# Kernel tuning notes

Hardware: AMD Instinct MI355X
Metric: run time of the kernel (lower is better)

## Reference

```python
import jax, jax.numpy as jnp
import numpy as np

B, S, D_IN, D_OUT = 4, 2048, 1024, 1024

def setup_inputs() -> dict:
    key = jax.random.key(0)
    ks = jax.random.split(key, 6)
    s = 1.0 / np.sqrt(D_IN)
    return {
        "inputs": jax.random.normal(ks[0], (B, S, D_IN), dtype=jnp.float32),
        "Wq": jax.random.normal(ks[1], (D_IN, D_OUT), dtype=jnp.float32) * s,
        "Wk": jax.random.normal(ks[2], (D_IN, D_OUT), dtype=jnp.float32) * s,
        "Wv": jax.random.normal(ks[3], (D_IN, D_OUT), dtype=jnp.float32) * s,
        "Wo": jax.random.normal(ks[4], (D_OUT, D_OUT), dtype=jnp.float32) * (1.0 / np.sqrt(D_OUT)),
        "bo": jax.random.normal(ks[5], (D_OUT,), dtype=jnp.float32) * 0.01,
    }

def reference(inputs, Wq, Wk, Wv, Wo, bo):
    # QKV projections (no bias, matching qkv_bias=False)
    q = inputs @ Wq  # [B,S,D]
    k = inputs @ Wk
    v = inputs @ Wv
    # naive full attention: scores [B,S,S]
    scores = jnp.einsum('bqd,bkd->bqk', q, k) / jnp.sqrt(jnp.asarray(k.shape[-1], q.dtype))
    attn = jax.nn.softmax(scores, axis=-1)
    out = jnp.einsum('bqk,bkd->bqd', attn, v)
    return out @ Wo + bo
```

## Files before the change

### kernel.cpp

```cpp
#include <hip/hip_runtime.h>
#include <hip/hip_bf16.h>
#include <cstdint>

typedef __attribute__((ext_vector_type(8))) __bf16 bf16x8;
typedef __attribute__((ext_vector_type(4))) float  f32x4;

__device__ __forceinline__ unsigned short f2bf(float x) {
    union { float f; unsigned u; } v; v.f = x;
    unsigned r = v.u + 0x7fffu + ((v.u >> 16) & 1u);
    return (unsigned short)(r >> 16);
}
__device__ __forceinline__ unsigned pack2bf(float a, float b) {
    return (unsigned)f2bf(a) | ((unsigned)f2bf(b) << 16);
}

__device__ __forceinline__ void gld_lds16(const unsigned short* g, unsigned short* l) {
    __builtin_amdgcn_global_load_lds(
        (const __attribute__((address_space(1))) unsigned int*)g,
        (__attribute__((address_space(3))) unsigned int*)l,
        16, 0, 0);
}

__global__ void cvt_kernel(const float* __restrict__ in, unsigned short* __restrict__ out, int n4) {
    int i = blockIdx.x * blockDim.x + threadIdx.x;
    if (i < n4) {
        float4 f = ((const float4*)in)[i];
        ushort4 o;
        o.x = f2bf(f.x); o.y = f2bf(f.y); o.z = f2bf(f.z); o.w = f2bf(f.w);
        ((ushort4*)out)[i] = o;
    }
}

__global__ void wpack_kernel(const float* __restrict__ W, unsigned short* __restrict__ out) {
    int tid  = threadIdx.x;
    int lane = tid & 63;
    int chunk = blockIdx.x * 4 + (tid >> 6);
    int nt = chunk >> 5, k32 = chunk & 31;
    int r = lane & 15, q = lane >> 4;
    const float* src = W + (size_t)(k32*32 + q*8) * 1024 + nt*16 + r;
    unsigned o[4];
#pragma unroll
    for (int i = 0; i < 4; i++)
        o[i] = pack2bf(src[(size_t)(2*i) * 1024], src[(size_t)(2*i+1) * 1024]);
    *(uint4*)(out + (size_t)chunk * 512 + lane * 8) = make_uint4(o[0], o[1], o[2], o[3]);
}

__global__ void softmax_kernel(unsigned short* __restrict__ S) {
    const size_t row = blockIdx.x;
    unsigned short* p = S + row * 2048;
    const int tid = threadIdx.x;
    const int wave = tid >> 6, lane = tid & 63;

    uint4 raw = ((const uint4*)p)[tid];
    unsigned u[4] = {raw.x, raw.y, raw.z, raw.w};
    float x[8];
#pragma unroll
    for (int i = 0; i < 4; i++) {
        x[2*i]   = __uint_as_float(u[i] << 16);
        x[2*i+1] = __uint_as_float(u[i] & 0xffff0000u);
    }
    float m = x[0];
#pragma unroll
    for (int i = 1; i < 8; i++) m = fmaxf(m, x[i]);
#pragma unroll
    for (int off = 32; off >= 1; off >>= 1) m = fmaxf(m, __shfl_xor(m, off, 64));
    __shared__ float sm[4], ss[4];
    if (lane == 0) sm[wave] = m;
    __syncthreads();
    m = fmaxf(fmaxf(sm[0], sm[1]), fmaxf(sm[2], sm[3]));

    float e[8], s = 0.f;
#pragma unroll
    for (int i = 0; i < 8; i++) { e[i] = __expf(x[i] - m); s += e[i]; }
#pragma unroll
    for (int off = 32; off >= 1; off >>= 1) s += __shfl_xor(s, off, 64);
    if (lane == 0) ss[wave] = s;
    __syncthreads();
    s = ss[0] + ss[1] + ss[2] + ss[3];
    float inv = 1.0f / s;

    unsigned o[4];
#pragma unroll
    for (int i = 0; i < 4; i++)
        o[i] = pack2bf(e[2*i] * inv, e[2*i+1] * inv);
    ((uint4*)p)[tid] = make_uint4(o[0], o[1], o[2], o[3]);
}

template<int EPI>
__global__ __launch_bounds__(256)
void gemm_pk(const unsigned short* __restrict__ A, const unsigned short* __restrict__ Bpk,
             void* __restrict__ C, unsigned short* __restrict__ Ck, unsigned short* __restrict__ Cv,
             const float* __restrict__ bias,
             int lda, int ldc, int KS, int nk2, float scale,
             long long sA, long long sB, long long sC)
{
    constexpr int SMEM = (EPI == 2) ? 34816 : 32768;
    __shared__ __align__(16) char smem[SMEM];

    const int tid  = threadIdx.x;
    const int lane = tid & 63;
    const int wave = tid >> 6;
    const int bz = blockIdx.z;
    A   += (size_t)bz * sA;
    Bpk += (size_t)bz * sB;
    const int bm = blockIdx.y * 128;
    const int bn = blockIdx.x * 128;

    const int srow = tid >> 2;
    const int scol = ((tid & 3) ^ ((tid >> 3) & 3)) * 8;
    const unsigned short* pa0 = A + (size_t)(bm + srow) * lda + scol;
    const unsigned short* pa1 = pa0 + 32;
    const unsigned short* pa2 = A + (size_t)(bm + 64 + srow) * lda + scol;
    const unsigned short* pa3 = pa2 + 32;

    const int wm = (wave & 1) * 64;
    const int wn = (wave >> 1) * 64;
    const int ln15 = lane & 15;
    const int quad = lane >> 4;
    const int fko = (quad ^ ((ln15 >> 1) & 3)) * 8;
    const int ldsoff = tid * 16;

    const unsigned short* pb[4];
#pragma unroll
    for (int j = 0; j < 4; j++)
        pb[j] = Bpk + (size_t)(((bn + wn + j*16) >> 4) * KS) * 512 + lane * 8;

    f32x4 acc[4][4];
#pragma unroll
    for (int i = 0; i < 4; i++)
#pragma unroll
        for (int j = 0; j < 4; j++) acc[i][j] = (f32x4){0.f, 0.f, 0.f, 0.f};

    auto stage_issue = [&](int p, bf16x8* br) {
        char* base = smem + p * 16384;
        gld_lds16(pa0, (unsigned short*)(base + ldsoff));
        gld_lds16(pa2, (unsigned short*)(base + 4096  + ldsoff));
        gld_lds16(pa1, (unsigned short*)(base + 8192  + ldsoff));
        gld_lds16(pa3, (unsigned short*)(base + 12288 + ldsoff));
        pa0 += 64; pa1 += 64; pa2 += 64; pa3 += 64;
#pragma unroll
        for (int j = 0; j < 4; j++) {
            br[j]     = *(const bf16x8*)(pb[j]);
            br[4 + j] = *(const bf16x8*)(pb[j] + 512);
            pb[j] += 1024;
        }
    };
    auto stage_compute = [&](int p, const bf16x8* br) {
        const unsigned short* As = (const unsigned short*)(smem + p * 16384);
#pragma unroll
        for (int t = 0; t < 2; t++) {
            bf16x8 af[4];
#pragma unroll
            for (int i = 0; i < 4; i++)
                af[i] = *(const bf16x8*)&As[t*4096 + (wm + i*16 + ln15) * 32 + fko];
#pragma unroll
            for (int i = 0; i < 4; i++)
#pragma unroll
                for (int j = 0; j < 4; j++)
                    acc[i][j] = __builtin_amdgcn_mfma_f32_16x16x32_bf16(
                        af[i], br[t*4 + j], acc[i][j], 0, 0, 0);
        }
    };

    bf16x8 b0[8], b1[8];
    stage_issue(0, b0);
    for (int kt = 0; kt < nk2; kt += 2) {
        asm volatile("s_waitcnt vmcnt(0)" ::: "memory");
        __syncthreads();
        stage_issue(1, b1);
        stage_compute(0, b0);
        asm volatile("s_waitcnt vmcnt(0)" ::: "memory");
        __syncthreads();
        if (kt + 2 < nk2) stage_issue(0, b0);
        stage_compute(1, b1);
    }

    if (EPI == 0) {
        float bval[4];
#pragma unroll
        for (int j = 0; j < 4; j++) bval[j] = bias[bn + wn + j*16 + ln15];
        float* Co = (float*)C + (size_t)bz * sC;
#pragma unroll
        for (int i = 0; i < 4; i++) {
            int r0 = bm + wm + i*16 + quad*4;
#pragma unroll
            for (int j = 0; j < 4; j++) {
                int c = bn + wn + j*16 + ln15;
#pragma unroll
                for (int r = 0; r < 4; r++)
                    Co[(size_t)(r0 + r) * ldc + c] = acc[i][j][r] * scale + bval[j];
            }
        }
    } else if (EPI == 1) {
        __syncthreads();
        float* ep = (float*)(smem + wave * 4352);
        unsigned short* Co = (unsigned short*)C + (size_t)bz * sC;
#pragma unroll
        for (int i = 0; i < 4; i++) {
#pragma unroll
            for (int j = 0; j < 4; j++)
#pragma unroll
                for (int r = 0; r < 4; r++)
                    ep[(quad*4 + r) * 68 + j*16 + ln15] = acc[i][j][r] * scale;
            __builtin_amdgcn_s_waitcnt(0);
#pragma unroll
            for (int p = 0; p < 2; p++) {
                int lrow = p*8 + (lane >> 3);
                int col0 = (lane & 7) * 8;
                float4 lo = *(const float4*)&ep[lrow * 68 + col0];
                float4 hi = *(const float4*)&ep[lrow * 68 + col0 + 4];
                uint4 o;
                o.x = pack2bf(lo.x, lo.y); o.y = pack2bf(lo.z, lo.w);
                o.z = pack2bf(hi.x, hi.y); o.w = pack2bf(hi.z, hi.w);
                *(uint4*)&Co[(size_t)(bm + wm + i*16 + lrow) * ldc + bn + wn + col0] = o;
            }
            __builtin_amdgcn_s_waitcnt(0);
        }
    } else {
        __syncthreads();
        float* ep = (float*)(smem + wave * 8704);
        const int region = bn >> 10;
#pragma unroll
        for (int half = 0; half < 2; half++) {
#pragma unroll
            for (int ii = 0; ii < 2; ii++) {
                int i = half*2 + ii;
#pragma unroll
                for (int j = 0; j < 4; j++)
#pragma unroll
                    for (int r = 0; r < 4; r++)
                        ep[(ii*16 + quad*4 + r) * 68 + j*16 + ln15] = acc[i][j][r] * scale;
            }
            __builtin_amdgcn_s_waitcnt(0);
            const int mrow0 = bm + wm + half*32;
            if (region == 0) {
                unsigned short* Q = (unsigned short*)C;
#pragma unroll
                for (int p = 0; p < 4; p++) {
                    int lrow = p*8 + (lane >> 3);
                    int col0 = (lane & 7) * 8;
                    float4 lo = *(const float4*)&ep[lrow * 68 + col0];
                    float4 hi = *(const float4*)&ep[lrow * 68 + col0 + 4];
                    uint4 o;
                    o.x = pack2bf(lo.x, lo.y); o.y = pack2bf(lo.z, lo.w);
                    o.z = pack2bf(hi.x, hi.y); o.w = pack2bf(hi.z, hi.w);
                    *(uint4*)&Q[(size_t)(mrow0 + lrow) * ldc + bn + wn + col0] = o;
                }
            } else if (region == 1) {
#pragma unroll
                for (int mt = 0; mt < 2; mt++)
#pragma unroll
                    for (int c = 0; c < 2; c++) {
                        float4 f0 = *(const float4*)&ep[(mt*16 + ln15) * 68 + c*32 + quad*8];
                        float4 f1 = *(const float4*)&ep[(mt*16 + ln15) * 68 + c*32 + quad*8 + 4];
                        uint4 o;
                        o.x = pack2bf(f0.x, f0.y); o.y = pack2bf(f0.z, f0.w);
                        o.z = pack2bf(f1.x, f1.y); o.w = pack2bf(f1.z, f1.w);
                        int cid = ((mrow0 + mt*16) >> 4) * 32 + ((bn - 1024 + wn + c*32) >> 5);
                        *(uint4*)(Ck + (size_t)cid * 512 + lane * 8) = o;
                    }
            } else {
                int s32 = mrow0 >> 5;
#pragma unroll
                for (int dt = 0; dt < 4; dt++) {
                    float v[8];
#pragma unroll
                    for (int e = 0; e < 8; e++)
                        v[e] = ep[(quad*8 + e) * 68 + dt*16 + ln15];
                    uint4 o;
                    o.x = pack2bf(v[0], v[1]); o.y = pack2bf(v[2], v[3]);
                    o.z = pack2bf(v[4], v[5]); o.w = pack2bf(v[6], v[7]);
                    int cid = (((bn - 2048 + wn) >> 4) + dt) * 256 + s32;
                    *(uint4*)(Cv + (size_t)cid * 512 + lane * 8) = o;
                }
            }
            __builtin_amdgcn_s_waitcnt(0);
        }
    }
}

extern "C" void kernel_launch(void* const* d_in, const int* in_sizes, int n_in,
                              void* d_out, int out_size, void* d_ws, size_t ws_size,
                              hipStream_t stream) {
    const float* X  = (const float*)d_in[0];
    const float* Wq = (const float*)d_in[1];
    const float* Wk = (const float*)d_in[2];
    const float* Wv = (const float*)d_in[3];
    const float* Wo = (const float*)d_in[4];
    const float* bo = (const float*)d_in[5];
    float* out = (float*)d_out;

    size_t off = 0;
    auto alloc = [&](size_t bytes) {
        void* p = (char*)d_ws + off;
        off += (bytes + 255) & ~(size_t)255;
        return p;
    };
    unsigned short* Xbf  = (unsigned short*)alloc(8192ull * 1024 * 2);
    unsigned short* Wpk  = (unsigned short*)alloc(192ull * 32 * 512 * 2);
    unsigned short* Wopk = (unsigned short*)alloc(64ull * 32 * 512 * 2);
    unsigned short* Qrm  = (unsigned short*)alloc(8192ull * 1024 * 2);
    unsigned short* Kpk  = (unsigned short*)alloc(512ull * 32 * 512 * 2);
    unsigned short* Vpk  = (unsigned short*)alloc(64ull * 256 * 512 * 2);
    unsigned short* Sc   = (unsigned short*)alloc(4ull * 2048 * 2048 * 2);
    unsigned short* AO   = Xbf;

    cvt_kernel<<<(8192*1024/4 + 255)/256, 256, 0, stream>>>(X, Xbf, 8192*1024/4);
    wpack_kernel<<<512, 256, 0, stream>>>(Wq, Wpk);
    wpack_kernel<<<512, 256, 0, stream>>>(Wk, Wpk + 64*32*512);
    wpack_kernel<<<512, 256, 0, stream>>>(Wv, Wpk + 128*32*512);
    wpack_kernel<<<512, 256, 0, stream>>>(Wo, Wopk);

    gemm_pk<2><<<dim3(3072/128, 8192/128, 1), 256, 0, stream>>>(
        Xbf, Wpk, Qrm, Kpk, Vpk, nullptr, 1024, 1024, 32, 16, 1.0f, 0, 0, 0);

    gemm_pk<1><<<dim3(2048/128, 2048/128, 4), 256, 0, stream>>>(
        Qrm, Kpk, Sc, nullptr, nullptr, nullptr, 1024, 2048, 32, 16, 0.03125f,
        2048ll*1024, 128ll*32*512, 2048ll*2048);

    softmax_kernel<<<8192, 256, 0, stream>>>(Sc);

    gemm_pk<1><<<dim3(1024/128, 2048/128, 4), 256, 0, stream>>>(
        Sc, Vpk, AO, nullptr, nullptr, nullptr, 2048, 1024, 256, 32, 1.0f,
        2048ll*2048, 64ll*512, 2048ll*1024);

    gemm_pk<0><<<dim3(1024/128, 8192/128, 1), 256, 0, stream>>>(
        AO, Wopk, out, nullptr, nullptr, bo, 1024, 1024, 32, 16, 1.0f, 0, 0, 0);

    (void)n_in; (void)in_sizes; (void)out_size; (void)ws_size;
}
```

Before: 304.3 us.

## Enlarge GEMM tiles to 256x128 with 512 threads, triple-buffered LDS pipeline and swizzled blocks

The GEMM kernel now uses 8 waves per block over a 256x128 output tile. A-tiles are loaded through a three-stage LDS ring buffer with partial vmcnt waits and split barriers, and MFMA sections are wrapped in s_setprio. Block indices are remapped with an 8-way swizzle to improve L2 reuse across neighbouring blocks. This aims to hide global-load latency and cut barrier stalls, at the cost of 96KB of LDS per block, which limits occupancy and may cause tail imbalance with fewer blocks.

```diff
diff --git a/kernel.cpp b/kernel.cpp
--- a/kernel.cpp
+++ b/kernel.cpp
@@ -87,15 +87,14 @@
 }
 
 template<int EPI>
-__global__ __launch_bounds__(256)
+__global__ __launch_bounds__(512, 2)
 void gemm_pk(const unsigned short* __restrict__ A, const unsigned short* __restrict__ Bpk,
              void* __restrict__ C, unsigned short* __restrict__ Ck, unsigned short* __restrict__ Cv,
              const float* __restrict__ bias,
-             int lda, int ldc, int KS, int nk2, float scale,
+             int lda, int ldc, int KS, int ns, float scale,
              long long sA, long long sB, long long sC)
 {
-    constexpr int SMEM = (EPI == 2) ? 34816 : 32768;
-    __shared__ __align__(16) char smem[SMEM];
+    __shared__ __align__(16) char smem[98304];
 
     const int tid  = threadIdx.x;
     const int lane = tid & 63;
@@ -103,21 +102,27 @@
     const int bz = blockIdx.z;
     A   += (size_t)bz * sA;
     Bpk += (size_t)bz * sB;
-    const int bm = blockIdx.y * 128;
-    const int bn = blockIdx.x * 128;
+
+    const int gx = gridDim.x;
+    int lin = blockIdx.y * gx + blockIdx.x;
+    int cpx = (gx * gridDim.y) >> 3;
+    int swz = (lin & 7) * cpx + (lin >> 3);
+    const int bm = (swz / gx) * 256;
+    const int bn = (swz % gx) * 128;
 
     const int srow = tid >> 2;
     const int scol = ((tid & 3) ^ ((tid >> 3) & 3)) * 8;
     const unsigned short* pa0 = A + (size_t)(bm + srow) * lda + scol;
     const unsigned short* pa1 = pa0 + 32;
-    const unsigned short* pa2 = A + (size_t)(bm + 64 + srow) * lda + scol;
+    const unsigned short* pa2 = A + (size_t)(bm + 128 + srow) * lda + scol;
     const unsigned short* pa3 = pa2 + 32;
 
-    const int wm = (wave & 1) * 64;
-    const int wn = (wave >> 1) * 64;
+    const int wm = (wave & 3) * 64;
+    const int wn = (wave >> 2) * 64;
     const int ln15 = lane & 15;
     const int quad = lane >> 4;
     const int fko = (quad ^ ((ln15 >> 1) & 3)) * 8;
+    const int rbase = (wm >> 7) * 4096 + (wm & 127) * 32;
     const int ldsoff = tid * 16;
 
     const unsigned short* pb[4];
@@ -131,13 +136,15 @@
 #pragma unroll
         for (int j = 0; j < 4; j++) acc[i][j] = (f32x4){0.f, 0.f, 0.f, 0.f};
 
-    auto stage_issue = [&](int p, bf16x8* br) {
-        char* base = smem + p * 16384;
+    auto dma = [&](int buf) {
+        char* base = smem + buf * 32768;
         gld_lds16(pa0, (unsigned short*)(base + ldsoff));
-        gld_lds16(pa2, (unsigned short*)(base + 4096  + ldsoff));
-        gld_lds16(pa1, (unsigned short*)(base + 8192  + ldsoff));
-        gld_lds16(pa3, (unsigned short*)(base + 12288 + ldsoff));
+        gld_lds16(pa2, (unsigned short*)(base + 8192  + ldsoff));
+        gld_lds16(pa1, (unsigned short*)(base + 16384 + ldsoff));
+        gld_lds16(pa3, (unsigned short*)(base + 24576 + ldsoff));
         pa0 += 64; pa1 += 64; pa2 += 64; pa3 += 64;
+    };
+    auto loadB = [&](bf16x8* br) {
 #pragma unroll
         for (int j = 0; j < 4; j++) {
             br[j]     = *(const bf16x8*)(pb[j]);
@@ -145,35 +152,53 @@
             pb[j] += 1024;
         }
     };
-    auto stage_compute = [&](int p, const bf16x8* br) {
-        const unsigned short* As = (const unsigned short*)(smem + p * 16384);
-#pragma unroll
-        for (int t = 0; t < 2; t++) {
-            bf16x8 af[4];
-#pragma unroll
-            for (int i = 0; i < 4; i++)
-                af[i] = *(const bf16x8*)&As[t*4096 + (wm + i*16 + ln15) * 32 + fko];
-#pragma unroll
-            for (int i = 0; i < 4; i++)
-#pragma unroll
-                for (int j = 0; j < 4; j++)
-                    acc[i][j] = __builtin_amdgcn_mfma_f32_16x16x32_bf16(
-                        af[i], br[t*4 + j], acc[i][j], 0, 0, 0);
-        }
+    auto phase = [&](const unsigned short* As, int t, const bf16x8* br) {
+        bf16x8 af[4];
+#pragma unroll
+        for (int i = 0; i < 4; i++)
+            af[i] = *(const bf16x8*)&As[t*8192 + rbase + i*512 + ln15*32 + fko];
+        __builtin_amdgcn_s_setprio(1);
+#pragma unroll
+        for (int i = 0; i < 4; i++)
+#pragma unroll
+            for (int j = 0; j < 4; j++)
+                acc[i][j] = __builtin_amdgcn_mfma_f32_16x16x32_bf16(
+                    af[i], br[t*4 + j], acc[i][j], 0, 0, 0);
+        __builtin_amdgcn_s_setprio(0);
     };
 
+#define SB __builtin_amdgcn_sched_barrier(0)
     bf16x8 b0[8], b1[8];
-    stage_issue(0, b0);
-    for (int kt = 0; kt < nk2; kt += 2) {
-        asm volatile("s_waitcnt vmcnt(0)" ::: "memory");
-        __syncthreads();
-        stage_issue(1, b1);
-        stage_compute(0, b0);
-        asm volatile("s_waitcnt vmcnt(0)" ::: "memory");
-        __syncthreads();
-        if (kt + 2 < nk2) stage_issue(0, b0);
-        stage_compute(1, b1);
+    SB; dma(0); SB; loadB(b0); SB; dma(1); SB;
+
+    int p = 0;
+    for (int it = 0; it < ns; it += 2) {
+        const unsigned short* As0 = (const unsigned short*)(smem + p * 32768);
+        int p1 = p + 1; if (p1 >= 3) p1 -= 3;
+        int q0 = p + 2; if (q0 >= 3) q0 -= 3;
+        const unsigned short* As1 = (const unsigned short*)(smem + p1 * 32768);
+        const bool more = (it + 2 < ns);
+
+        asm volatile("s_waitcnt vmcnt(12)" ::: "memory");
+        SB; __builtin_amdgcn_s_barrier(); SB;
+        loadB(b1); SB;
+        phase(As0, 0, b0);
+        __builtin_amdgcn_s_barrier(); SB;
+        if (more) { dma(q0); SB; }
+        phase(As0, 1, b0);
+
+        if (more) { asm volatile("s_waitcnt vmcnt(12)" ::: "memory"); }
+        else      { asm volatile("s_waitcnt vmcnt(8)"  ::: "memory"); }
+        SB; __builtin_amdgcn_s_barrier(); SB;
+        if (more) { loadB(b0); SB; }
+        phase(As1, 0, b1);
+        __builtin_amdgcn_s_barrier(); SB;
+        if (it + 3 < ns) { dma(p); SB; }
+        phase(As1, 1, b1);
+
+        p = q0;
     }
+#undef SB
 
     if (EPI == 0) {
         float bval[4];
@@ -204,8 +229,8 @@
                     ep[(quad*4 + r) * 68 + j*16 + ln15] = acc[i][j][r] * scale;
             __builtin_amdgcn_s_waitcnt(0);
 #pragma unroll
-            for (int p = 0; p < 2; p++) {
-                int lrow = p*8 + (lane >> 3);
+            for (int pp = 0; pp < 2; pp++) {
+                int lrow = pp*8 + (lane >> 3);
                 int col0 = (lane & 7) * 8;
                 float4 lo = *(const float4*)&ep[lrow * 68 + col0];
                 float4 hi = *(const float4*)&ep[lrow * 68 + col0 + 4];
@@ -236,8 +261,8 @@
             if (region == 0) {
                 unsigned short* Q = (unsigned short*)C;
 #pragma unroll
-                for (int p = 0; p < 4; p++) {
-                    int lrow = p*8 + (lane >> 3);
+                for (int pp = 0; pp < 4; pp++) {
+                    int lrow = pp*8 + (lane >> 3);
                     int col0 = (lane & 7) * 8;
                     float4 lo = *(const float4*)&ep[lrow * 68 + col0];
                     float4 hi = *(const float4*)&ep[lrow * 68 + col0 + 4];
@@ -311,20 +336,20 @@
     wpack_kernel<<<512, 256, 0, stream>>>(Wv, Wpk + 128*32*512);
     wpack_kernel<<<512, 256, 0, stream>>>(Wo, Wopk);
 
-    gemm_pk<2><<<dim3(3072/128, 8192/128, 1), 256, 0, stream>>>(
+    gemm_pk<2><<<dim3(3072/128, 8192/256, 1), 512, 0, stream>>>(
         Xbf, Wpk, Qrm, Kpk, Vpk, nullptr, 1024, 1024, 32, 16, 1.0f, 0, 0, 0);
 
-    gemm_pk<1><<<dim3(2048/128, 2048/128, 4), 256, 0, stream>>>(
+    gemm_pk<1><<<dim3(2048/128, 2048/256, 4), 512, 0, stream>>>(
         Qrm, Kpk, Sc, nullptr, nullptr, nullptr, 1024, 2048, 32, 16, 0.03125f,
         2048ll*1024, 128ll*32*512, 2048ll*2048);
 
     softmax_kernel<<<8192, 256, 0, stream>>>(Sc);
 
-    gemm_pk<1><<<dim3(1024/128, 2048/128, 4), 256, 0, stream>>>(
+    gemm_pk<1><<<dim3(1024/128, 2048/256, 4), 512, 0, stream>>>(
         Sc, Vpk, AO, nullptr, nullptr, nullptr, 2048, 1024, 256, 32, 1.0f,
         2048ll*2048, 64ll*512, 2048ll*1024);
 
-    gemm_pk<0><<<dim3(1024/128, 8192/128, 1), 256, 0, stream>>>(
+    gemm_pk<0><<<dim3(1024/128, 8192/256, 1), 512, 0, stream>>>(
         AO, Wopk, out, nullptr, nullptr, bo, 1024, 1024, 32, 16, 1.0f, 0, 0, 0);
 
     (void)n_in; (void)in_sizes; (void)out_size; (void)ws_size;
```

After: 301.9 us. About the same (-0.8%).
